# Optimization experiments

Measured on AMD Instinct MI355X. Metric: run time of the kernel, lower is better.

Reference implementation:

```python
import jax, jax.numpy as jnp
import numpy as np

H = 512          # hidden_size
F = 2048         # intermediate_size
E = 16           # n_routed_experts
SHARED = 2       # n_shared_experts
TOP_K = 4        # n_activated_experts
B, S = 2, 2048


def _mlp(x, w1, b1, w2, b2):
    # Standard MLP: Linear -> GELU(exact) -> Linear (dropout inactive at eval)
    return jax.nn.gelu(x @ w1 + b1, approximate=False) @ w2 + b2


def setup_inputs() -> dict:
    key = jax.random.key(0)
    ks = jax.random.split(key, 10)
    sc = 0.02
    return {
        "hidden_states": jax.random.normal(ks[0], (B, S, H), dtype=jnp.float32),
        "gate_w": jax.random.normal(ks[1], (E, H), dtype=jnp.float32) * sc,  # nn.Linear weight [out,in], no bias
        "re_w1": jax.random.normal(ks[2], (E, H, F), dtype=jnp.float32) * sc,
        "re_b1": jnp.zeros((E, F), dtype=jnp.float32),
        "re_w2": jax.random.normal(ks[3], (E, F, H), dtype=jnp.float32) * sc,
        "re_b2": jnp.zeros((E, H), dtype=jnp.float32),
        "se_w1": jax.random.normal(ks[4], (SHARED, H, F), dtype=jnp.float32) * sc,
        "se_b1": jnp.zeros((SHARED, F), dtype=jnp.float32),
        "se_w2": jax.random.normal(ks[5], (SHARED, F, H), dtype=jnp.float32) * sc,
        "se_b2": jnp.zeros((SHARED, H), dtype=jnp.float32),
    }


def reference(hidden_states, gate_w, re_w1, re_b1, re_w2, re_b2,
              se_w1, se_b1, se_w2, se_b2):
    b, s, h = hidden_states.shape
    x = hidden_states.reshape(-1, h)                       # [T, H]
    # --- gating: softmax -> top-k -> renormalize over top-k ---
    gate_probs = jax.nn.softmax(x @ gate_w.T, axis=-1)     # [T, E]
    top_v, top_i = jax.lax.top_k(gate_probs, TOP_K)        # [T, K]
    top_v = jax.nn.softmax(top_v, axis=-1)
    # combine weights per expert: zero for non-selected experts (same math as masked scatter-add)
    combine = jnp.einsum('tk,tke->te', top_v,
                         jax.nn.one_hot(top_i, E, dtype=x.dtype))  # [T, E]
    # --- routed experts (weight is 0 for tokens not routed to expert e) ---
    routed = jnp.zeros_like(x)
    for e in range(E):
        routed = routed + combine[:, e:e + 1] * _mlp(x, re_w1[e], re_b1[e], re_w2[e], re_b2[e])
    # --- shared experts: average ---
    shared = jnp.zeros_like(x)
    for j in range(SHARED):
        shared = shared + _mlp(x, se_w1[j], se_b1[j], se_w2[j], se_b2[j])
    shared = shared / SHARED
    return (routed + shared).reshape(b, s, h)
```

## Files before the change

### kernel.cpp

```cpp
#include <hip/hip_runtime.h>

#define T_TOK 4096
#define H_DIM 512
#define F_DIM 2048
#define N_EXP 16
#define N_SH  2
#define TOPK  4

typedef __attribute__((ext_vector_type(4))) float f32x4;
typedef __attribute__((ext_vector_type(8))) short bf16x8;

__device__ __forceinline__ unsigned short f2bf(float f){
  union { float f; unsigned u; } a; a.f = f;
  unsigned u = a.u;
  return (unsigned short)((u + 0x7fffu + ((u >> 16) & 1u)) >> 16);
}

#define GLD16(gsrc, ldst) \
  __builtin_amdgcn_global_load_lds((const __attribute__((address_space(1))) unsigned int*)(gsrc), \
                                   (__attribute__((address_space(3))) unsigned int*)(ldst), 16, 0, 0)

__global__ void moe_convert_x(const float4* __restrict__ src, ushort4* __restrict__ dst){
  int i = blockIdx.x * 256 + threadIdx.x;
  float4 v = src[i];
  ushort4 o;
  o.x = f2bf(v.x); o.y = f2bf(v.y); o.z = f2bf(v.z); o.w = f2bf(v.w);
  dst[i] = o;
}

__global__ void moe_transpose(const float* __restrict__ src, unsigned short* __restrict__ dst,
                              int R, int C){
  __shared__ float tile[64][65];
  size_t matoff = (size_t)blockIdx.z * (size_t)R * (size_t)C;
  src += matoff; dst += matoff;
  int c0 = blockIdx.x * 64, r0 = blockIdx.y * 64;
  int t = threadIdx.x;
  #pragma unroll
  for (int i = 0; i < 16; ++i){
    int idx = i * 256 + t; int r = idx >> 6, c = idx & 63;
    tile[r][c] = src[(size_t)(r0 + r) * C + (c0 + c)];
  }
  __syncthreads();
  #pragma unroll
  for (int i = 0; i < 16; ++i){
    int idx = i * 256 + t; int r = idx >> 6, c = idx & 63;
    dst[(size_t)(c0 + r) * R + (r0 + c)] = f2bf(tile[c][r]);
  }
}

__global__ __launch_bounds__(256) void moe_gate(
    const float* __restrict__ x, const float* __restrict__ gw,
    int* __restrict__ tki, float* __restrict__ tkw,
    int* __restrict__ counts){
  __shared__ float gwl[N_EXP * H_DIM];
  int tid = threadIdx.x;
  #pragma unroll
  for (int i = 0; i < N_EXP * H_DIM / 256; ++i)
    gwl[i * 256 + tid] = gw[i * 256 + tid];
  __syncthreads();

  int t = blockIdx.x * 256 + tid;
  const float4* xr = (const float4*)(x + (size_t)t * H_DIM);
  float acc[N_EXP];
  #pragma unroll
  for (int e = 0; e < N_EXP; ++e) acc[e] = 0.f;
  for (int h4 = 0; h4 < H_DIM / 4; ++h4){
    float4 xv = xr[h4];
    #pragma unroll
    for (int e = 0; e < N_EXP; ++e){
      const float* wrow = &gwl[e * H_DIM + h4 * 4];
      acc[e] += xv.x * wrow[0] + xv.y * wrow[1] + xv.z * wrow[2] + xv.w * wrow[3];
    }
  }
  float m = -1e30f;
  #pragma unroll
  for (int e = 0; e < N_EXP; ++e) m = fmaxf(m, acc[e]);
  float Z = 0.f;
  #pragma unroll
  for (int e = 0; e < N_EXP; ++e){ acc[e] = __expf(acc[e] - m); Z += acc[e]; }
  float inv = 1.f / Z;
  #pragma unroll
  for (int e = 0; e < N_EXP; ++e) acc[e] *= inv;
  int sel[TOPK]; float sv[TOPK];
  unsigned used = 0;
  #pragma unroll
  for (int k = 0; k < TOPK; ++k){
    int best = 0; float bv = -1.f;
    #pragma unroll
    for (int e = 0; e < N_EXP; ++e)
      if (!((used >> e) & 1u) && acc[e] > bv){ bv = acc[e]; best = e; }
    used |= 1u << best; sel[k] = best; sv[k] = bv;
  }
  float m0 = sv[0];
  float Z2 = 0.f;
  #pragma unroll
  for (int k = 0; k < TOPK; ++k){ sv[k] = __expf(sv[k] - m0); Z2 += sv[k]; }
  float i2 = 1.f / Z2;
  #pragma unroll
  for (int k = 0; k < TOPK; ++k){
    tki[t * TOPK + k] = sel[k];
    tkw[t * TOPK + k] = sv[k] * i2;
    atomicAdd(&counts[sel[k]], 1);
  }
}

__global__ void moe_offsets(const int* __restrict__ counts, int* __restrict__ offs,
                            int* __restrict__ cursor){
  if (threadIdx.x == 0){
    int a = 0;
    for (int e = 0; e < N_EXP; ++e){ offs[e] = a; cursor[e] = a; a += counts[e]; }
  }
}

__global__ void moe_build_rows(const int* __restrict__ tki, const float* __restrict__ tkw,
                               int* __restrict__ cursor, int* __restrict__ rows,
                               float* __restrict__ roww){
  int t = blockIdx.x * 256 + threadIdx.x;
  if (t >= T_TOK) return;
  for (int k = 0; k < TOPK; ++k){
    int e = tki[t * TOPK + k];
    int pos = atomicAdd(&cursor[e], 1);
    rows[pos] = t;
    roww[pos] = tkw[t * TOPK + k];
  }
}

__global__ __launch_bounds__(256, 2) void moe_gemm1(
    const unsigned short* __restrict__ xb,
    const unsigned short* __restrict__ rw1T,
    const unsigned short* __restrict__ sw1T,
    const float* __restrict__ rb1, const float* __restrict__ sb1,
    const int* __restrict__ counts, const int* __restrict__ offs,
    const int* __restrict__ rows,
    unsigned short* __restrict__ h_rout, unsigned short* __restrict__ h_sh){
  constexpr int K  = H_DIM;
  constexpr int NK = K / 64;
  int job = blockIdx.z;
  int M; const int* rmap; const unsigned short* wT; const float* bias; unsigned short* hout;
  if (job < N_EXP){
    M = counts[job];
    int base = offs[job];
    rmap = rows + base;
    wT = rw1T + (size_t)job * F_DIM * H_DIM;
    bias = rb1 + job * F_DIM;
    hout = h_rout + (size_t)base * F_DIM;
  } else {
    int s = job - N_EXP;
    M = T_TOK; rmap = nullptr;
    wT = sw1T + (size_t)s * F_DIM * H_DIM;
    bias = sb1 + s * F_DIM;
    hout = h_sh + (size_t)s * T_TOK * F_DIM;
  }
  int m0 = blockIdx.y * 128;
  if (m0 >= M) return;
  int n0 = blockIdx.x * 128;

  __shared__ char smem[65536];
  int tid = threadIdx.x;
  int wave = tid >> 6, lane = tid & 63;
  int wm = wave >> 1, wn = wave & 1;

  const unsigned short* asrc[4];
  const unsigned short* bsrc[4];
  int srow = tid >> 3;
  int slot = tid & 7;
  #pragma unroll
  for (int r = 0; r < 4; ++r){
    int row = r * 32 + srow;
    int gr = m0 + row; if (gr > M - 1) gr = M - 1;
    int tok = rmap ? rmap[gr] : gr;
    asrc[r] = xb + (size_t)tok * H_DIM + ((slot ^ (row & 7)) << 3);
    bsrc[r] = wT + (size_t)(n0 + row) * K + ((slot ^ (row & 7)) << 3);
  }

  f32x4 acc[4][4];
  #pragma unroll
  for (int i = 0; i < 4; ++i)
    #pragma unroll
    for (int j = 0; j < 4; ++j) acc[i][j] = (f32x4)0.f;

  auto stage = [&](int buf, int k0){
    char* base = smem + buf * 32768;
    #pragma unroll
    for (int r = 0; r < 4; ++r) GLD16(asrc[r] + k0, base + r * 4096 + wave * 1024);
    #pragma unroll
    for (int r = 0; r < 4; ++r) GLD16(bsrc[r] + k0, base + 16384 + r * 4096 + wave * 1024);
  };

  stage(0, 0);
  int buf = 0;
  for (int kt = 0; kt < NK; ++kt){
    __syncthreads();
    if (kt + 1 < NK) stage(buf ^ 1, (kt + 1) * 64);
    const char* A = smem + buf * 32768;
    const char* B = A + 16384;
    #pragma unroll
    for (int ks = 0; ks < 2; ++ks){
      int kg = ks * 4 + (lane >> 4);
      bf16x8 a[4], b[4];
      #pragma unroll
      for (int f = 0; f < 4; ++f){
        int row = wm * 64 + f * 16 + (lane & 15);
        a[f] = *(const bf16x8*)(A + row * 128 + ((kg ^ (row & 7)) << 4));
      }
      #pragma unroll
      for (int f = 0; f < 4; ++f){
        int row = wn * 64 + f * 16 + (lane & 15);
        b[f] = *(const bf16x8*)(B + row * 128 + ((kg ^ (row & 7)) << 4));
      }
      #pragma unroll
      for (int fm = 0; fm < 4; ++fm)
        #pragma unroll
        for (int fn = 0; fn < 4; ++fn)
          acc[fm][fn] = __builtin_amdgcn_mfma_f32_16x16x32_bf16(a[fm], b[fn], acc[fm][fn], 0, 0, 0);
    }
    buf ^= 1;
  }

  #pragma unroll
  for (int fm = 0; fm < 4; ++fm){
    #pragma unroll
    for (int j = 0; j < 4; ++j){
      int row = wm * 64 + fm * 16 + (lane >> 4) * 4 + j;
      int gr = m0 + row;
      if (gr < M){
        #pragma unroll
        for (int fn = 0; fn < 4; ++fn){
          int col = n0 + wn * 64 + fn * 16 + (lane & 15);
          float v = acc[fm][fn][j] + bias[col];
          v = 0.5f * v * (1.0f + erff(v * 0.70710678118654752f));
          hout[(size_t)gr * F_DIM + col] = f2bf(v);
        }
      }
    }
  }
}

__global__ __launch_bounds__(256, 2) void moe_gemm2(
    const unsigned short* __restrict__ h_rout,
    const unsigned short* __restrict__ h_sh,
    const unsigned short* __restrict__ rw2T,
    const unsigned short* __restrict__ sw2T,
    const float* __restrict__ rb2, const float* __restrict__ sb2,
    const int* __restrict__ counts, const int* __restrict__ offs,
    const int* __restrict__ rows, const float* __restrict__ roww,
    float* __restrict__ out){
  constexpr int K  = F_DIM;
  constexpr int NK = K / 64;
  int job = blockIdx.z;
  int M; const unsigned short* aseg; const unsigned short* wT; const float* bias;
  const int* rmap; const float* rwt;
  if (job < N_EXP){
    M = counts[job];
    int base = offs[job];
    aseg = h_rout + (size_t)base * F_DIM;
    rmap = rows + base; rwt = roww + base;
    wT = rw2T + (size_t)job * H_DIM * F_DIM;
    bias = rb2 + job * H_DIM;
  } else {
    int s = job - N_EXP; M = T_TOK;
    aseg = h_sh + (size_t)s * T_TOK * F_DIM;
    rmap = nullptr; rwt = nullptr;
    wT = sw2T + (size_t)s * H_DIM * F_DIM;
    bias = sb2 + s * H_DIM;
  }
  int m0 = blockIdx.y * 128;
  if (m0 >= M) return;
  int n0 = blockIdx.x * 128;

  __shared__ char smem[65536];
  int tid = threadIdx.x;
  int wave = tid >> 6, lane = tid & 63;
  int wm = wave >> 1, wn = wave & 1;

  const unsigned short* asrc[4];
  const unsigned short* bsrc[4];
  int srow = tid >> 3;
  int slot = tid & 7;
  #pragma unroll
  for (int r = 0; r < 4; ++r){
    int row = r * 32 + srow;
    int gr = m0 + row; if (gr > M - 1) gr = M - 1;
    asrc[r] = aseg + (size_t)gr * K + ((slot ^ (row & 7)) << 3);
    bsrc[r] = wT + (size_t)(n0 + row) * K + ((slot ^ (row & 7)) << 3);
  }

  f32x4 acc[4][4];
  #pragma unroll
  for (int i = 0; i < 4; ++i)
    #pragma unroll
    for (int j = 0; j < 4; ++j) acc[i][j] = (f32x4)0.f;

  auto stage = [&](int buf, int k0){
    char* base = smem + buf * 32768;
    #pragma unroll
    for (int r = 0; r < 4; ++r) GLD16(asrc[r] + k0, base + r * 4096 + wave * 1024);
    #pragma unroll
    for (int r = 0; r < 4; ++r) GLD16(bsrc[r] + k0, base + 16384 + r * 4096 + wave * 1024);
  };

  stage(0, 0);
  int buf = 0;
  for (int kt = 0; kt < NK; ++kt){
    __syncthreads();
    if (kt + 1 < NK) stage(buf ^ 1, (kt + 1) * 64);
    const char* A = smem + buf * 32768;
    const char* B = A + 16384;
    #pragma unroll
    for (int ks = 0; ks < 2; ++ks){
      int kg = ks * 4 + (lane >> 4);
      bf16x8 a[4], b[4];
      #pragma unroll
      for (int f = 0; f < 4; ++f){
        int row = wm * 64 + f * 16 + (lane & 15);
        a[f] = *(const bf16x8*)(A + row * 128 + ((kg ^ (row & 7)) << 4));
      }
      #pragma unroll
      for (int f = 0; f < 4; ++f){
        int row = wn * 64 + f * 16 + (lane & 15);
        b[f] = *(const bf16x8*)(B + row * 128 + ((kg ^ (row & 7)) << 4));
      }
      #pragma unroll
      for (int fm = 0; fm < 4; ++fm)
        #pragma unroll
        for (int fn = 0; fn < 4; ++fn)
          acc[fm][fn] = __builtin_amdgcn_mfma_f32_16x16x32_bf16(a[fm], b[fn], acc[fm][fn], 0, 0, 0);
    }
    buf ^= 1;
  }

  #pragma unroll
  for (int fm = 0; fm < 4; ++fm){
    #pragma unroll
    for (int j = 0; j < 4; ++j){
      int row = wm * 64 + fm * 16 + (lane >> 4) * 4 + j;
      int gr = m0 + row;
      if (gr < M){
        int tok; float coef;
        if (rmap){ tok = rmap[gr]; coef = rwt[gr]; }
        else     { tok = gr;       coef = 1.0f / N_SH; }
        #pragma unroll
        for (int fn = 0; fn < 4; ++fn){
          int col = n0 + wn * 64 + fn * 16 + (lane & 15);
          float v = (acc[fm][fn][j] + bias[col]) * coef;
          atomicAdd(&out[(size_t)tok * H_DIM + col], v);
        }
      }
    }
  }
}

extern "C" void kernel_launch(void* const* d_in, const int* in_sizes, int n_in,
                              void* d_out, int out_size, void* d_ws, size_t ws_size,
                              hipStream_t stream){
  const float* x   = (const float*)d_in[0];
  const float* gw  = (const float*)d_in[1];
  const float* rw1 = (const float*)d_in[2];
  const float* rb1 = (const float*)d_in[3];
  const float* rw2 = (const float*)d_in[4];
  const float* rb2 = (const float*)d_in[5];
  const float* sw1 = (const float*)d_in[6];
  const float* sb1 = (const float*)d_in[7];
  const float* sw2 = (const float*)d_in[8];
  const float* sb2 = (const float*)d_in[9];
  float* out = (float*)d_out;

  char* ws = (char*)d_ws;
  size_t off = 0;
  auto alloc = [&](size_t b){ size_t r = off; off += (b + 255) & ~(size_t)255; return r; };
  unsigned short* xb     = (unsigned short*)(ws + alloc((size_t)T_TOK * H_DIM * 2));
  unsigned short* rw1T   = (unsigned short*)(ws + alloc((size_t)N_EXP * H_DIM * F_DIM * 2));
  unsigned short* rw2T   = (unsigned short*)(ws + alloc((size_t)N_EXP * H_DIM * F_DIM * 2));
  unsigned short* sw1T   = (unsigned short*)(ws + alloc((size_t)N_SH * H_DIM * F_DIM * 2));
  unsigned short* sw2T   = (unsigned short*)(ws + alloc((size_t)N_SH * H_DIM * F_DIM * 2));
  unsigned short* h_rout = (unsigned short*)(ws + alloc((size_t)T_TOK * TOPK * F_DIM * 2));
  unsigned short* h_sh   = (unsigned short*)(ws + alloc((size_t)N_SH * T_TOK * F_DIM * 2));
  int*   counts = (int*)(ws + alloc(64));
  int*   offs   = (int*)(ws + alloc(64));
  int*   cursor = (int*)(ws + alloc(64));
  int*   tki    = (int*)(ws + alloc((size_t)T_TOK * TOPK * 4));
  float* tkw    = (float*)(ws + alloc((size_t)T_TOK * TOPK * 4));
  int*   rowsl  = (int*)(ws + alloc((size_t)T_TOK * TOPK * 4));
  float* roww   = (float*)(ws + alloc((size_t)T_TOK * TOPK * 4));

  hipMemsetAsync(counts, 0, 64, stream);
  hipMemsetAsync(out, 0, (size_t)T_TOK * H_DIM * 4, stream);

  moe_convert_x<<<2048, 256, 0, stream>>>((const float4*)x, (ushort4*)xb);
  moe_transpose<<<dim3(F_DIM / 64, H_DIM / 64, N_EXP), 256, 0, stream>>>(rw1, rw1T, H_DIM, F_DIM);
  moe_transpose<<<dim3(H_DIM / 64, F_DIM / 64, N_EXP), 256, 0, stream>>>(rw2, rw2T, F_DIM, H_DIM);
  moe_transpose<<<dim3(F_DIM / 64, H_DIM / 64, N_SH), 256, 0, stream>>>(sw1, sw1T, H_DIM, F_DIM);
  moe_transpose<<<dim3(H_DIM / 64, F_DIM / 64, N_SH), 256, 0, stream>>>(sw2, sw2T, F_DIM, H_DIM);

  moe_gate<<<T_TOK / 256, 256, 0, stream>>>(x, gw, tki, tkw, counts);
  moe_offsets<<<1, 64, 0, stream>>>(counts, offs, cursor);
  moe_build_rows<<<T_TOK / 256, 256, 0, stream>>>(tki, tkw, cursor, rowsl, roww);

  moe_gemm1<<<dim3(F_DIM / 128, T_TOK / 128, N_EXP + N_SH), 256, 0, stream>>>(
      xb, rw1T, sw1T, rb1, sb1, counts, offs, rowsl, h_rout, h_sh);
  moe_gemm2<<<dim3(H_DIM / 128, T_TOK / 128, N_EXP + N_SH), 256, 0, stream>>>(
      h_rout, h_sh, rw2T, sw2T, rb2, sb2, counts, offs, rowsl, roww, out);
}
```

Before: 582.3 us.

## Single-buffer GEMM smem for higher occupancy, fuse x conversion into gate, tanh GELU

Both MoE GEMM kernels move from a double-buffered 64KB LDS pipeline to a single 32KB buffer with launch bounds raised to 4 blocks per CU. The aim is to hide latency through occupancy instead of software prefetch. The bf16 conversion of x is folded into the gating kernel, and the four weight-transpose launches are merged into two. The exact erf GELU is replaced by a tanh approximation built on exp/rcp, which changes numerics slightly. Dropping the prefetch adds an extra barrier per K step and exposes load latency if occupancy does not rise.

New measurement: 542.3 us. -6.9%, faster.

```diff
diff --git a/kernel.cpp b/kernel.cpp
--- a/kernel.cpp
+++ b/kernel.cpp
@@ -16,23 +16,26 @@
   return (unsigned short)((u + 0x7fffu + ((u >> 16) & 1u)) >> 16);
 }
 
+__device__ __forceinline__ float fast_gelu(float v){
+  float u = 0.7978845608f * (v + 0.044715f * v * v * v);
+  u = fminf(fmaxf(u, -15.f), 15.f);
+  float e = __expf(2.f * u);
+  float th = (e - 1.f) * __builtin_amdgcn_rcpf(e + 1.f);
+  return 0.5f * v * (1.f + th);
+}
+
 #define GLD16(gsrc, ldst) \
   __builtin_amdgcn_global_load_lds((const __attribute__((address_space(1))) unsigned int*)(gsrc), \
                                    (__attribute__((address_space(3))) unsigned int*)(ldst), 16, 0, 0)
 
-__global__ void moe_convert_x(const float4* __restrict__ src, ushort4* __restrict__ dst){
-  int i = blockIdx.x * 256 + threadIdx.x;
-  float4 v = src[i];
-  ushort4 o;
-  o.x = f2bf(v.x); o.y = f2bf(v.y); o.z = f2bf(v.z); o.w = f2bf(v.w);
-  dst[i] = o;
-}
-
-__global__ void moe_transpose(const float* __restrict__ src, unsigned short* __restrict__ dst,
-                              int R, int C){
+__global__ void moe_transpose2(const float* __restrict__ s0, const float* __restrict__ s1,
+                               unsigned short* __restrict__ d0, unsigned short* __restrict__ d1,
+                               int R, int C){
   __shared__ float tile[64][65];
-  size_t matoff = (size_t)blockIdx.z * (size_t)R * (size_t)C;
-  src += matoff; dst += matoff;
+  int z = blockIdx.z;
+  size_t per = (size_t)R * C;
+  const float* src      = (z < N_EXP) ? s0 + (size_t)z * per : s1 + (size_t)(z - N_EXP) * per;
+  unsigned short* dst   = (z < N_EXP) ? d0 + (size_t)z * per : d1 + (size_t)(z - N_EXP) * per;
   int c0 = blockIdx.x * 64, r0 = blockIdx.y * 64;
   int t = threadIdx.x;
   #pragma unroll
@@ -50,6 +53,7 @@
 
 __global__ __launch_bounds__(256) void moe_gate(
     const float* __restrict__ x, const float* __restrict__ gw,
+    unsigned short* __restrict__ xb,
     int* __restrict__ tki, float* __restrict__ tkw,
     int* __restrict__ counts){
   __shared__ float gwl[N_EXP * H_DIM];
@@ -61,11 +65,14 @@
 
   int t = blockIdx.x * 256 + tid;
   const float4* xr = (const float4*)(x + (size_t)t * H_DIM);
+  ushort4* xw = (ushort4*)(xb + (size_t)t * H_DIM);
   float acc[N_EXP];
   #pragma unroll
   for (int e = 0; e < N_EXP; ++e) acc[e] = 0.f;
   for (int h4 = 0; h4 < H_DIM / 4; ++h4){
     float4 xv = xr[h4];
+    ushort4 o; o.x = f2bf(xv.x); o.y = f2bf(xv.y); o.z = f2bf(xv.z); o.w = f2bf(xv.w);
+    xw[h4] = o;
     #pragma unroll
     for (int e = 0; e < N_EXP; ++e){
       const float* wrow = &gwl[e * H_DIM + h4 * 4];
@@ -125,7 +132,7 @@
   }
 }
 
-__global__ __launch_bounds__(256, 2) void moe_gemm1(
+__global__ __launch_bounds__(256, 4) void moe_gemm1(
     const unsigned short* __restrict__ xb,
     const unsigned short* __restrict__ rw1T,
     const unsigned short* __restrict__ sw1T,
@@ -155,7 +162,7 @@
   if (m0 >= M) return;
   int n0 = blockIdx.x * 128;
 
-  __shared__ char smem[65536];
+  __shared__ char smem[32768];
   int tid = threadIdx.x;
   int wave = tid >> 6, lane = tid & 63;
   int wm = wave >> 1, wn = wave & 1;
@@ -179,20 +186,18 @@
     #pragma unroll
     for (int j = 0; j < 4; ++j) acc[i][j] = (f32x4)0.f;
 
-  auto stage = [&](int buf, int k0){
-    char* base = smem + buf * 32768;
-    #pragma unroll
-    for (int r = 0; r < 4; ++r) GLD16(asrc[r] + k0, base + r * 4096 + wave * 1024);
-    #pragma unroll
-    for (int r = 0; r < 4; ++r) GLD16(bsrc[r] + k0, base + 16384 + r * 4096 + wave * 1024);
+  auto stage = [&](int k0){
+    #pragma unroll
+    for (int r = 0; r < 4; ++r) GLD16(asrc[r] + k0, smem + r * 4096 + wave * 1024);
+    #pragma unroll
+    for (int r = 0; r < 4; ++r) GLD16(bsrc[r] + k0, smem + 16384 + r * 4096 + wave * 1024);
   };
 
-  stage(0, 0);
-  int buf = 0;
   for (int kt = 0; kt < NK; ++kt){
+    if (kt) __syncthreads();
+    stage(kt * 64);
     __syncthreads();
-    if (kt + 1 < NK) stage(buf ^ 1, (kt + 1) * 64);
-    const char* A = smem + buf * 32768;
+    const char* A = smem;
     const char* B = A + 16384;
     #pragma unroll
     for (int ks = 0; ks < 2; ++ks){
@@ -214,7 +219,6 @@
         for (int fn = 0; fn < 4; ++fn)
           acc[fm][fn] = __builtin_amdgcn_mfma_f32_16x16x32_bf16(a[fm], b[fn], acc[fm][fn], 0, 0, 0);
     }
-    buf ^= 1;
   }
 
   #pragma unroll
@@ -228,15 +232,14 @@
         for (int fn = 0; fn < 4; ++fn){
           int col = n0 + wn * 64 + fn * 16 + (lane & 15);
           float v = acc[fm][fn][j] + bias[col];
-          v = 0.5f * v * (1.0f + erff(v * 0.70710678118654752f));
-          hout[(size_t)gr * F_DIM + col] = f2bf(v);
+          hout[(size_t)gr * F_DIM + col] = f2bf(fast_gelu(v));
         }
       }
     }
   }
 }
 
-__global__ __launch_bounds__(256, 2) void moe_gemm2(
+__global__ __launch_bounds__(256, 4) void moe_gemm2(
     const unsigned short* __restrict__ h_rout,
     const unsigned short* __restrict__ h_sh,
     const unsigned short* __restrict__ rw2T,
@@ -268,7 +271,7 @@
   if (m0 >= M) return;
   int n0 = blockIdx.x * 128;
 
-  __shared__ char smem[65536];
+  __shared__ char smem[32768];
   int tid = threadIdx.x;
   int wave = tid >> 6, lane = tid & 63;
   int wm = wave >> 1, wn = wave & 1;
@@ -291,20 +294,18 @@
     #pragma unroll
     for (int j = 0; j < 4; ++j) acc[i][j] = (f32x4)0.f;
 
-  auto stage = [&](int buf, int k0){
-    char* base = smem + buf * 32768;
-    #pragma unroll
-    for (int r = 0; r < 4; ++r) GLD16(asrc[r] + k0, base + r * 4096 + wave * 1024);
-    #pragma unroll
-    for (int r = 0; r < 4; ++r) GLD16(bsrc[r] + k0, base + 16384 + r * 4096 + wave * 1024);
+  auto stage = [&](int k0){
+    #pragma unroll
+    for (int r = 0; r < 4; ++r) GLD16(asrc[r] + k0, smem + r * 4096 + wave * 1024);
+    #pragma unroll
+    for (int r = 0; r < 4; ++r) GLD16(bsrc[r] + k0, smem + 16384 + r * 4096 + wave * 1024);
   };
 
-  stage(0, 0);
-  int buf = 0;
   for (int kt = 0; kt < NK; ++kt){
+    if (kt) __syncthreads();
+    stage(kt * 64);
     __syncthreads();
-    if (kt + 1 < NK) stage(buf ^ 1, (kt + 1) * 64);
-    const char* A = smem + buf * 32768;
+    const char* A = smem;
     const char* B = A + 16384;
     #pragma unroll
     for (int ks = 0; ks < 2; ++ks){
@@ -326,7 +327,6 @@
         for (int fn = 0; fn < 4; ++fn)
           acc[fm][fn] = __builtin_amdgcn_mfma_f32_16x16x32_bf16(a[fm], b[fn], acc[fm][fn], 0, 0, 0);
     }
-    buf ^= 1;
   }
 
   #pragma unroll
@@ -386,13 +386,13 @@
   hipMemsetAsync(counts, 0, 64, stream);
   hipMemsetAsync(out, 0, (size_t)T_TOK * H_DIM * 4, stream);
 
-  moe_convert_x<<<2048, 256, 0, stream>>>((const float4*)x, (ushort4*)xb);
-  moe_transpose<<<dim3(F_DIM / 64, H_DIM / 64, N_EXP), 256, 0, stream>>>(rw1, rw1T, H_DIM, F_DIM);
-  moe_transpose<<<dim3(H_DIM / 64, F_DIM / 64, N_EXP), 256, 0, stream>>>(rw2, rw2T, F_DIM, H_DIM);
-  moe_transpose<<<dim3(F_DIM / 64, H_DIM / 64, N_SH), 256, 0, stream>>>(sw1, sw1T, H_DIM, F_DIM);
-  moe_transpose<<<dim3(H_DIM / 64, F_DIM / 64, N_SH), 256, 0, stream>>>(sw2, sw2T, F_DIM, H_DIM);
-
-  moe_gate<<<T_TOK / 256, 256, 0, stream>>>(x, gw, tki, tkw, counts);
+  moe_gate<<<T_TOK / 256, 256, 0, stream>>>(x, gw, xb, tki, tkw, counts);
+
+  moe_transpose2<<<dim3(F_DIM / 64, H_DIM / 64, N_EXP + N_SH), 256, 0, stream>>>(
+      rw1, sw1, rw1T, sw1T, H_DIM, F_DIM);
+  moe_transpose2<<<dim3(H_DIM / 64, F_DIM / 64, N_EXP + N_SH), 256, 0, stream>>>(
+      rw2, sw2, rw2T, sw2T, F_DIM, H_DIM);
+
   moe_offsets<<<1, 64, 0, stream>>>(counts, offs, cursor);
   moe_build_rows<<<T_TOK / 256, 256, 0, stream>>>(tki, tkw, cursor, rowsl, roww);
 
```
